# Performance work log

Measured on AMD Instinct MI355X. Metric: run time of the kernel, lower is better.

## Reference

```python
import jax, jax.numpy as jnp
import numpy as np

L, B, D, A, H = 128, 128, 1024, 1024, 2048  # src_len, batch, dec_hid, align, enc_hid


def setup_inputs() -> dict:
    key = jax.random.key(0)
    ks = jax.random.split(key, 8)
    s_tm1 = jax.random.normal(ks[0], (B, D), dtype=jnp.float32)
    xs_h = jax.random.normal(ks[1], (L, B, H), dtype=jnp.float32)
    uh = jax.random.normal(ks[2], (L, B, A), dtype=jnp.float32)
    xs_mask = jnp.ones((L, B), dtype=jnp.float32)
    # learned params: sa = Linear(D -> A), a1 = Linear(A -> 1)
    W_sa = jax.random.normal(ks[3], (A, D), dtype=jnp.float32) * 0.02
    b_sa = jnp.zeros((A,), dtype=jnp.float32)
    w_a1 = jax.random.normal(ks[4], (A,), dtype=jnp.float32) * 0.02
    b_a1 = jnp.zeros((), dtype=jnp.float32)
    return {"s_tm1": s_tm1, "xs_h": xs_h, "uh": uh, "xs_mask": xs_mask,
            "W_sa": W_sa, "b_sa": b_sa, "w_a1": w_a1, "b_a1": b_a1}


def reference(s_tm1, xs_h, uh, xs_mask, W_sa, b_sa, w_a1, b_a1):
    # sa(s_tm1): (B, A), broadcast over L against uh (L, B, A)
    proj = s_tm1 @ W_sa.T + b_sa
    h = jnp.tanh(proj[None, :, :] + uh)            # (L, B, A)
    # a1: (L, B, A) . (A,) -> (L, B); exp (no max-subtraction, faithful to source)
    e_ij = jnp.exp(jnp.einsum('lba,a->lb', h, w_a1) + b_a1)
    e_ij = e_ij * xs_mask
    e_ij = e_ij / e_ij.sum(axis=0, keepdims=True)  # normalize over source length
    attend = jnp.einsum('lb,lbh->bh', e_ij, xs_h)  # (B, H)
    return e_ij, attend
```

## Files before the change

kernel.cpp:

```cpp
#include <hip/hip_runtime.h>

#define L_DIM 128
#define B_DIM 128
#define D_DIM 1024
#define A_DIM 1024
#define H_DIM 2048
#define KSPLIT 16

__global__ __launch_bounds__(256) void k1_gemm_part(const float* __restrict__ s_tm1,
                                                    const float* __restrict__ W_sa,
                                                    float* __restrict__ proj_part) {
    __shared__ float sWT[64][68];
    __shared__ float sST[64][68];
    const int a0 = blockIdx.x * 64;
    const int b0 = blockIdx.y * 64;
    const int kc = blockIdx.z;
    const int k0 = kc * 64;
    const int t  = threadIdx.x;

    {
        const int c = (t & 15) * 4;
        const int r = t >> 4;
#pragma unroll
        for (int p = 0; p < 4; ++p) {
            const int row = r + p * 16;
            float4 w4 = *(const float4*)(W_sa + (size_t)(a0 + row) * D_DIM + k0 + c);
            sWT[c + 0][row] = w4.x; sWT[c + 1][row] = w4.y;
            sWT[c + 2][row] = w4.z; sWT[c + 3][row] = w4.w;
            float4 s4 = *(const float4*)(s_tm1 + (size_t)(b0 + row) * D_DIM + k0 + c);
            sST[c + 0][row] = s4.x; sST[c + 1][row] = s4.y;
            sST[c + 2][row] = s4.z; sST[c + 3][row] = s4.w;
        }
    }
    __syncthreads();

    const int tx = t & 15;
    const int ty = t >> 4;
    float acc[4][4] = {};
#pragma unroll 4
    for (int d = 0; d < 64; ++d) {
        float4 av = *(const float4*)&sWT[d][tx * 4];
        float4 bv = *(const float4*)&sST[d][ty * 4];
        float a_[4] = {av.x, av.y, av.z, av.w};
        float b_[4] = {bv.x, bv.y, bv.z, bv.w};
#pragma unroll
        for (int j = 0; j < 4; ++j)
#pragma unroll
            for (int i = 0; i < 4; ++i)
                acc[j][i] += a_[i] * b_[j];
    }

    float* base = proj_part + (size_t)kc * B_DIM * A_DIM;
#pragma unroll
    for (int j = 0; j < 4; ++j)
#pragma unroll
        for (int i = 0; i < 4; ++i)
            base[(size_t)(b0 + ty * 4 + j) * A_DIM + a0 + tx * 4 + i] = acc[j][i];
}

__global__ __launch_bounds__(256) void k1_reduce(const float* __restrict__ proj_part,
                                                 float* __restrict__ proj) {
    const size_t i4 = (size_t)blockIdx.x * 256 + threadIdx.x;
    const float4* pp = (const float4*)proj_part;
    float4 acc = pp[i4];
#pragma unroll
    for (int kc = 1; kc < KSPLIT; ++kc) {
        float4 v = pp[(size_t)kc * (B_DIM * A_DIM / 4) + i4];
        acc.x += v.x; acc.y += v.y; acc.z += v.z; acc.w += v.w;
    }
    ((float4*)proj)[i4] = acc;
}

__device__ __forceinline__ float tanh_fast(float x) {
    float e = __expf(2.0f * x);
    return (e - 1.0f) * __builtin_amdgcn_rcpf(e + 1.0f);
}

__global__ __launch_bounds__(256) void k2_logits(const float* __restrict__ uh,
                                                 const float* __restrict__ proj,
                                                 const float* __restrict__ b_sa,
                                                 const float* __restrict__ w_a1,
                                                 const float* __restrict__ b_a1,
                                                 const float* __restrict__ mask,
                                                 float* __restrict__ e_raw) {
    const int wave = threadIdx.x >> 6;
    const int lane = threadIdx.x & 63;
    const int flat = blockIdx.x * 4 + wave;
    const int b    = flat & (B_DIM - 1);

    const float* up = uh   + (size_t)flat * A_DIM;
    const float* pp = proj + (size_t)b    * A_DIM;

    float acc = 0.0f;
#pragma unroll
    for (int c = 0; c < 4; ++c) {
        const int off = c * 256 + lane * 4;
        float4 u = *(const float4*)(up + off);
        float4 p = *(const float4*)(pp + off);
        float4 s = *(const float4*)(b_sa + off);
        float4 w = *(const float4*)(w_a1 + off);
        acc += tanh_fast(u.x + p.x + s.x) * w.x;
        acc += tanh_fast(u.y + p.y + s.y) * w.y;
        acc += tanh_fast(u.z + p.z + s.z) * w.z;
        acc += tanh_fast(u.w + p.w + s.w) * w.w;
    }
#pragma unroll
    for (int off = 32; off > 0; off >>= 1)
        acc += __shfl_down(acc, off);
    if (lane == 0)
        e_raw[flat] = __expf(acc + b_a1[0]) * mask[flat];
}

__global__ __launch_bounds__(256) void k3_attend(const float* __restrict__ e_raw,
                                                 const float* __restrict__ xs_h,
                                                 float* __restrict__ out_e,
                                                 float* __restrict__ out_att) {
    __shared__ float se[L_DIM];
    __shared__ float s_inv;
    const int b     = blockIdx.y;
    const int chunk = blockIdx.x;
    const int t     = threadIdx.x;

    if (t < L_DIM) se[t] = e_raw[t * B_DIM + b];
    __syncthreads();
    if (t < 64) {
        float v = se[t] + se[t + 64];
#pragma unroll
        for (int off = 32; off > 0; off >>= 1)
            v += __shfl_down(v, off);
        if (t == 0) s_inv = 1.0f / v;
    }
    __syncthreads();
    if (t < L_DIM) se[t] *= s_inv;
    __syncthreads();
    if (chunk == 0 && t < L_DIM) out_e[t * B_DIM + b] = se[t];

    const int h0 = chunk * 512 + t * 2;
    const float* xp = xs_h + (size_t)b * H_DIM + h0;
    float accx = 0.0f, accy = 0.0f;
#pragma unroll 8
    for (int l = 0; l < L_DIM; ++l) {
        float  w = se[l];
        float2 x = *(const float2*)(xp + (size_t)l * (B_DIM * H_DIM));
        accx += w * x.x;
        accy += w * x.y;
    }
    float* op = out_att + (size_t)b * H_DIM + h0;
    op[0] = accx;
    op[1] = accy;
}

extern "C" void kernel_launch(void* const* d_in, const int* in_sizes, int n_in,
                              void* d_out, int out_size, void* d_ws, size_t ws_size,
                              hipStream_t stream) {
    const float* s_tm1 = (const float*)d_in[0];
    const float* xs_h  = (const float*)d_in[1];
    const float* uh    = (const float*)d_in[2];
    const float* mask  = (const float*)d_in[3];
    const float* W_sa  = (const float*)d_in[4];
    const float* b_sa  = (const float*)d_in[5];
    const float* w_a1  = (const float*)d_in[6];
    const float* b_a1  = (const float*)d_in[7];

    float* proj_part = (float*)d_ws;
    float* proj      = proj_part + (size_t)KSPLIT * B_DIM * A_DIM;
    float* e_raw     = proj + (size_t)B_DIM * A_DIM;

    float* out_e   = (float*)d_out;
    float* out_att = out_e + L_DIM * B_DIM;

    k1_gemm_part<<<dim3(A_DIM / 64, B_DIM / 64, KSPLIT), 256, 0, stream>>>(
        s_tm1, W_sa, proj_part);
    k1_reduce<<<dim3(B_DIM * A_DIM / 4 / 256), 256, 0, stream>>>(proj_part, proj);
    k2_logits<<<dim3(L_DIM * B_DIM / 4), 256, 0, stream>>>(uh, proj, b_sa, w_a1,
                                                           b_a1, mask, e_raw);
    k3_attend<<<dim3(H_DIM / 512, B_DIM), 256, 0, stream>>>(e_raw, xs_h,
                                                            out_e, out_att);
}
```

Measured before the change: 256.7 us.

## Fuse split-K reduction into logits kernel and reduce K-split count

The GEMM's K split drops from 16 to 4, each block looping over four 64-wide K chunks and writing partials with float4 stores. The separate reduce kernel is removed. The logits kernel now sums the partials when it loads proj, and each wave reuses that projection across four rows of L. This removes one launch and the write and re-read of the 16 partial buffers, but the GEMM has fewer blocks and the logits grid shrinks to 1024 blocks.

```diff
diff --git a/kernel.cpp b/kernel.cpp
--- a/kernel.cpp
+++ b/kernel.cpp
@@ -5,7 +5,7 @@
 #define D_DIM 1024
 #define A_DIM 1024
 #define H_DIM 2048
-#define KSPLIT 16
+#define KSPLIT 4
 
 __global__ __launch_bounds__(256) void k1_gemm_part(const float* __restrict__ s_tm1,
                                                     const float* __restrict__ W_sa,
@@ -15,12 +15,16 @@
     const int a0 = blockIdx.x * 64;
     const int b0 = blockIdx.y * 64;
     const int kc = blockIdx.z;
-    const int k0 = kc * 64;
     const int t  = threadIdx.x;
+    const int c  = (t & 15) * 4;
+    const int r  = t >> 4;
+    const int tx = t & 15;
+    const int ty = t >> 4;
 
-    {
-        const int c = (t & 15) * 4;
-        const int r = t >> 4;
+    float acc[4][4] = {};
+
+    for (int kk = 0; kk < 4; ++kk) {
+        const int k0 = kc * 256 + kk * 64;
 #pragma unroll
         for (int p = 0; p < 4; ++p) {
             const int row = r + p * 16;
@@ -31,44 +35,29 @@
             sST[c + 0][row] = s4.x; sST[c + 1][row] = s4.y;
             sST[c + 2][row] = s4.z; sST[c + 3][row] = s4.w;
         }
-    }
-    __syncthreads();
+        __syncthreads();
 
-    const int tx = t & 15;
-    const int ty = t >> 4;
-    float acc[4][4] = {};
 #pragma unroll 4
-    for (int d = 0; d < 64; ++d) {
-        float4 av = *(const float4*)&sWT[d][tx * 4];
-        float4 bv = *(const float4*)&sST[d][ty * 4];
-        float a_[4] = {av.x, av.y, av.z, av.w};
-        float b_[4] = {bv.x, bv.y, bv.z, bv.w};
+        for (int d = 0; d < 64; ++d) {
+            float4 av = *(const float4*)&sWT[d][tx * 4];
+            float4 bv = *(const float4*)&sST[d][ty * 4];
+            float a_[4] = {av.x, av.y, av.z, av.w};
+            float b_[4] = {bv.x, bv.y, bv.z, bv.w};
 #pragma unroll
-        for (int j = 0; j < 4; ++j)
+            for (int j = 0; j < 4; ++j)
 #pragma unroll
-            for (int i = 0; i < 4; ++i)
-                acc[j][i] += a_[i] * b_[j];
+                for (int i = 0; i < 4; ++i)
+                    acc[j][i] += a_[i] * b_[j];
+        }
+        __syncthreads();
     }
 
     float* base = proj_part + (size_t)kc * B_DIM * A_DIM;
 #pragma unroll
-    for (int j = 0; j < 4; ++j)
-#pragma unroll
-        for (int i = 0; i < 4; ++i)
-            base[(size_t)(b0 + ty * 4 + j) * A_DIM + a0 + tx * 4 + i] = acc[j][i];
-}
-
-__global__ __launch_bounds__(256) void k1_reduce(const float* __restrict__ proj_part,
-                                                 float* __restrict__ proj) {
-    const size_t i4 = (size_t)blockIdx.x * 256 + threadIdx.x;
-    const float4* pp = (const float4*)proj_part;
-    float4 acc = pp[i4];
-#pragma unroll
-    for (int kc = 1; kc < KSPLIT; ++kc) {
-        float4 v = pp[(size_t)kc * (B_DIM * A_DIM / 4) + i4];
-        acc.x += v.x; acc.y += v.y; acc.z += v.z; acc.w += v.w;
+    for (int j = 0; j < 4; ++j) {
+        float4 v = {acc[j][0], acc[j][1], acc[j][2], acc[j][3]};
+        *(float4*)(base + (size_t)(b0 + ty * 4 + j) * A_DIM + a0 + tx * 4) = v;
     }
-    ((float4*)proj)[i4] = acc;
 }
 
 __device__ __forceinline__ float tanh_fast(float x) {
@@ -77,38 +66,52 @@
 }
 
 __global__ __launch_bounds__(256) void k2_logits(const float* __restrict__ uh,
-                                                 const float* __restrict__ proj,
+                                                 const float* __restrict__ proj_part,
                                                  const float* __restrict__ b_sa,
                                                  const float* __restrict__ w_a1,
                                                  const float* __restrict__ b_a1,
                                                  const float* __restrict__ mask,
                                                  float* __restrict__ e_raw) {
-    const int wave = threadIdx.x >> 6;
-    const int lane = threadIdx.x & 63;
-    const int flat = blockIdx.x * 4 + wave;
-    const int b    = flat & (B_DIM - 1);
+    const int wave_g = blockIdx.x * 4 + (threadIdx.x >> 6);
+    const int lane   = threadIdx.x & 63;
+    const int b      = wave_g & (B_DIM - 1);
 
-    const float* up = uh   + (size_t)flat * A_DIM;
-    const float* pp = proj + (size_t)b    * A_DIM;
-
-    float acc = 0.0f;
+    float4 p[4], s[4], w[4];
 #pragma unroll
     for (int c = 0; c < 4; ++c) {
         const int off = c * 256 + lane * 4;
-        float4 u = *(const float4*)(up + off);
-        float4 p = *(const float4*)(pp + off);
-        float4 s = *(const float4*)(b_sa + off);
-        float4 w = *(const float4*)(w_a1 + off);
-        acc += tanh_fast(u.x + p.x + s.x) * w.x;
-        acc += tanh_fast(u.y + p.y + s.y) * w.y;
-        acc += tanh_fast(u.z + p.z + s.z) * w.z;
-        acc += tanh_fast(u.w + p.w + s.w) * w.w;
+        p[c] = *(const float4*)(proj_part + (size_t)b * A_DIM + off);
+#pragma unroll
+        for (int kc = 1; kc < KSPLIT; ++kc) {
+            float4 v = *(const float4*)(proj_part +
+                (size_t)kc * B_DIM * A_DIM + (size_t)b * A_DIM + off);
+            p[c].x += v.x; p[c].y += v.y; p[c].z += v.z; p[c].w += v.w;
+        }
+        s[c] = *(const float4*)(b_sa + off);
+        w[c] = *(const float4*)(w_a1 + off);
     }
+    const float ba1 = b_a1[0];
+
 #pragma unroll
-    for (int off = 32; off > 0; off >>= 1)
-        acc += __shfl_down(acc, off);
-    if (lane == 0)
-        e_raw[flat] = __expf(acc + b_a1[0]) * mask[flat];
+    for (int j = 0; j < 4; ++j) {
+        const int flat = wave_g + j * 4096;
+        const float* up = uh + (size_t)flat * A_DIM;
+        float acc = 0.0f;
+#pragma unroll
+        for (int c = 0; c < 4; ++c) {
+            const int off = c * 256 + lane * 4;
+            float4 u = *(const float4*)(up + off);
+            acc += tanh_fast(u.x + p[c].x + s[c].x) * w[c].x;
+            acc += tanh_fast(u.y + p[c].y + s[c].y) * w[c].y;
+            acc += tanh_fast(u.z + p[c].z + s[c].z) * w[c].z;
+            acc += tanh_fast(u.w + p[c].w + s[c].w) * w[c].w;
+        }
+#pragma unroll
+        for (int off = 32; off > 0; off >>= 1)
+            acc += __shfl_down(acc, off);
+        if (lane == 0)
+            e_raw[flat] = __expf(acc + ba1) * mask[flat];
+    }
 }
 
 __global__ __launch_bounds__(256) void k3_attend(const float* __restrict__ e_raw,
@@ -163,17 +166,15 @@
     const float* b_a1  = (const float*)d_in[7];
 
     float* proj_part = (float*)d_ws;
-    float* proj      = proj_part + (size_t)KSPLIT * B_DIM * A_DIM;
-    float* e_raw     = proj + (size_t)B_DIM * A_DIM;
+    float* e_raw     = proj_part + (size_t)KSPLIT * B_DIM * A_DIM;
 
     float* out_e   = (float*)d_out;
     float* out_att = out_e + L_DIM * B_DIM;
 
     k1_gemm_part<<<dim3(A_DIM / 64, B_DIM / 64, KSPLIT), 256, 0, stream>>>(
         s_tm1, W_sa, proj_part);
-    k1_reduce<<<dim3(B_DIM * A_DIM / 4 / 256), 256, 0, stream>>>(proj_part, proj);
-    k2_logits<<<dim3(L_DIM * B_DIM / 4), 256, 0, stream>>>(uh, proj, b_sa, w_a1,
-                                                           b_a1, mask, e_raw);
+    k2_logits<<<dim3(1024), 256, 0, stream>>>(uh, proj_part, b_sa, w_a1,
+                                              b_a1, mask, e_raw);
     k3_attend<<<dim3(H_DIM / 512, B_DIM), 256, 0, stream>>>(e_raw, xs_h,
                                                             out_e, out_att);
 }
```

Measured after the change: 262.4 us. +2.2%, slower.
